# Optimization experiments

Hardware: AMD Instinct MI355X
Metric: run time of the kernel (lower is better)

## Reference

```python
import jax, jax.numpy as jnp
import numpy as np

DIM = 512
NUM_HEADS = 8
HEAD_DIM = DIM // NUM_HEADS


def setup_inputs() -> dict:
    key = jax.random.key(0)
    k1, k2, k3, k4 = jax.random.split(key, 4)
    B, N = 8, 32 * 32
    x = jax.random.normal(k1, (B, N, DIM), dtype=jnp.float32)
    # nn.Linear(dim, 3*dim, bias=False): weight [3*dim, dim], y = x @ W.T
    w_qkv = jax.random.normal(k2, (3 * DIM, DIM), dtype=jnp.float32) * 0.02
    w_proj = jax.random.normal(k3, (DIM, DIM), dtype=jnp.float32) * 0.02
    log_decay = jnp.zeros((NUM_HEADS,), dtype=jnp.float32)
    return {"x": x, "w_qkv": w_qkv, "w_proj": w_proj, "log_decay": log_decay,
            "H": 32, "W": 32}


def _manhattan_dist(H: int, W: int) -> jnp.ndarray:
    # [H*W, H*W] Manhattan distance between grid positions
    rows = jnp.repeat(jnp.arange(H), W)  # [N]
    cols = jnp.tile(jnp.arange(W), H)    # [N]
    dist = (jnp.abs(rows[:, None] - rows[None, :])
            + jnp.abs(cols[:, None] - cols[None, :]))
    return dist.astype(jnp.float32)


def reference(x, w_qkv, w_proj, log_decay, H, W):
    B, N, C = x.shape
    nh, hd = NUM_HEADS, HEAD_DIM
    scale = hd ** -0.5
    qkv = jnp.einsum('bnc,dc->bnd', x, w_qkv)          # [B, N, 3C]
    qkv = qkv.reshape(B, N, 3, nh, hd).transpose(2, 0, 3, 1, 4)
    q, k, v = qkv[0], qkv[1], qkv[2]                   # [B, nh, N, hd]
    attn = jnp.einsum('bhid,bhjd->bhij', q, k) * scale  # [B, nh, N, N]
    dist = _manhattan_dist(H, W)                        # [N, N]
    decay = jax.nn.softplus(log_decay)                  # [nh]
    bias = -decay[:, None, None] * dist[None]           # [nh, N, N]
    attn = jax.nn.softmax(attn + bias[None], axis=-1)
    out = jnp.einsum('bhij,bhjd->bhid', attn, v)        # [B, nh, N, hd]
    out = out.transpose(0, 2, 1, 3).reshape(B, N, C)
    return jnp.einsum('bnc,dc->bnd', out, w_proj)


if __name__ == "__main__":
    out = reference(**setup_inputs())
    print(out.shape, out.dtype)
```

## Files before the change

### kernel.cpp

```cpp
#include <hip/hip_runtime.h>
#include <stdint.h>

typedef _Float16 f16;
typedef _Float16 f16x8 __attribute__((ext_vector_type(8)));
typedef _Float16 f16x4 __attribute__((ext_vector_type(4)));
typedef float f32x4 __attribute__((ext_vector_type(4)));

#define MROWS 8192
#define KDIM 512
#define NSEQ 1024
#define NH 8

__device__ __forceinline__ void gload16(void* lds, const void* g) {
  __builtin_amdgcn_global_load_lds(
      (const __attribute__((address_space(1))) unsigned*)g,
      (__attribute__((address_space(3))) unsigned*)lds, 16, 0, 0);
}

__device__ __forceinline__ f32x4 mfma16(f16x8 a, f16x8 b, f32x4 c) {
  return __builtin_amdgcn_mfma_f32_16x16x32_f16(a, b, c, 0, 0, 0);
}

__device__ __forceinline__ int vsg(int d) {
  return ((d >> 1) & 7) ^ ((d & 1) << 2);
}

__global__ __launch_bounds__(256) void cvt_kernel(
    const float* __restrict__ x, const float* __restrict__ wq,
    const float* __restrict__ wp, f16* __restrict__ x16,
    f16* __restrict__ wq16, f16* __restrict__ wp16) {
  int t = blockIdx.x * 256 + threadIdx.x;
  int stride = gridDim.x * 256;
  for (int i = t; i < (MROWS * KDIM) / 4; i += stride) {
    float4 v = ((const float4*)x)[i];
    f16x4 o = {(f16)v.x, (f16)v.y, (f16)v.z, (f16)v.w};
    ((f16x4*)x16)[i] = o;
  }
  for (int i = t; i < (3 * KDIM * KDIM) / 4; i += stride) {
    float4 v = ((const float4*)wq)[i];
    f16x4 o = {(f16)v.x, (f16)v.y, (f16)v.z, (f16)v.w};
    ((f16x4*)wq16)[i] = o;
  }
  for (int i = t; i < (KDIM * KDIM) / 4; i += stride) {
    float4 v = ((const float4*)wp)[i];
    f16x4 o = {(f16)v.x, (f16)v.y, (f16)v.z, (f16)v.w};
    ((f16x4*)wp16)[i] = o;
  }
}

__device__ __forceinline__ void gemm_mainloop_db(
    const f16* __restrict__ A, const f16* __restrict__ B, int m0, int n0,
    f16* As0, f16* As1, f16* Bs0, f16* Bs1, f32x4 (&acc)[4][4]) {
  const int tid = threadIdx.x;
  const int w = tid >> 6, l = tid & 63;
  const int wr = w >> 1, wc = w & 1;
  const int lrow = l & 15, lk = l >> 4;
  const int srow = l >> 3, sslot = l & 7;
  const int scol = ((sslot ^ srow) << 3);
  const int NT = KDIM / 64;

  auto STAGE = [&](int bb, int kb) {
    f16* Ad = bb ? As1 : As0;
    f16* Bd = bb ? Bs1 : Bs0;
#pragma unroll
    for (int j = 0; j < 4; ++j) {
      int i = w * 4 + j;
      int row = i * 8 + srow;
      gload16(Ad + i * 512, A + (size_t)(m0 + row) * KDIM + kb + scol);
      gload16(Bd + i * 512, B + (size_t)(n0 + row) * KDIM + kb + scol);
    }
  };

  STAGE(0, 0);
#pragma unroll 1
  for (int t = 0; t < NT; ++t) {
    if (t + 1 < NT) {
      STAGE((t + 1) & 1, (t + 1) * 64);
      asm volatile("s_waitcnt vmcnt(8)" ::: "memory");
    } else {
      asm volatile("s_waitcnt vmcnt(0)" ::: "memory");
    }
    __builtin_amdgcn_s_barrier();
    const f16* Asr = (t & 1) ? As1 : As0;
    const f16* Bsr = (t & 1) ? Bs1 : Bs0;
#pragma unroll
    for (int kk = 0; kk < 2; ++kk) {
      int slotbase = kk * 4 + lk;
      f16x8 af[4], bf[4];
#pragma unroll
      for (int mi = 0; mi < 4; ++mi) {
        int row = wr * 64 + mi * 16 + lrow;
        af[mi] = *(const f16x8*)(Asr + row * 64 + ((slotbase ^ (row & 7)) << 3));
      }
#pragma unroll
      for (int nj = 0; nj < 4; ++nj) {
        int row = wc * 64 + nj * 16 + lrow;
        bf[nj] = *(const f16x8*)(Bsr + row * 64 + ((slotbase ^ (row & 7)) << 3));
      }
#pragma unroll
      for (int mi = 0; mi < 4; ++mi)
#pragma unroll
        for (int nj = 0; nj < 4; ++nj)
          acc[mi][nj] = mfma16(af[mi], bf[nj], acc[mi][nj]);
    }
    __builtin_amdgcn_s_barrier();
  }
}

__global__ __launch_bounds__(256, 2) void qkv_gemm(
    const f16* __restrict__ x16, const f16* __restrict__ wq16,
    f16* __restrict__ q16, f16* __restrict__ k16, f16* __restrict__ v16T) {
  __shared__ f16 SMEM[4 * 128 * 64];
  f16* As0 = SMEM;
  f16* As1 = SMEM + 8192;
  f16* Bs0 = SMEM + 16384;
  f16* Bs1 = SMEM + 24576;

  f32x4 acc[4][4];
#pragma unroll
  for (int i = 0; i < 4; ++i)
#pragma unroll
    for (int j = 0; j < 4; ++j) acc[i][j] = (f32x4){0.f, 0.f, 0.f, 0.f};

  const int m0 = blockIdx.y * 128, n0 = blockIdx.x * 128;
  gemm_mainloop_db(x16, wq16, m0, n0, As0, As1, Bs0, Bs1, acc);

  const int tid = threadIdx.x;
  const int w = tid >> 6, l = tid & 63;
  const int wr = w >> 1, wc = w & 1;
  const int lrow = l & 15, lk = l >> 4;

  if (n0 < 1024) {
#pragma unroll
    for (int mi = 0; mi < 4; ++mi) {
#pragma unroll
      for (int rr = 0; rr < 4; ++rr) {
        int m = m0 + wr * 64 + mi * 16 + lk * 4 + rr;
        int b = m >> 10, n = m & 1023;
#pragma unroll
        for (int nj = 0; nj < 4; ++nj) {
          int d = n0 + wc * 64 + nj * 16 + lrow;
          int which = d >> 9, c = d & 511;
          int h = c >> 6, dd = c & 63;
          f16 val = (f16)acc[mi][nj][rr];
          size_t hb = (size_t)(b * NH + h);
          if (which == 0)
            q16[(hb * NSEQ + n) * 64 + dd] = val;
          else
            k16[(hb * NSEQ + n) * 64 + dd] = val;
        }
      }
    }
  } else {
    f16* T = SMEM;
#pragma unroll
    for (int mi = 0; mi < 4; ++mi) {
#pragma unroll
      for (int nj = 0; nj < 4; ++nj) {
        int dloc = wc * 64 + nj * 16 + lrow;
        int nloc = wr * 64 + mi * 16 + lk * 4;
        f16x4 pw = {(f16)acc[mi][nj][0], (f16)acc[mi][nj][1],
                    (f16)acc[mi][nj][2], (f16)acc[mi][nj][3]};
        *(f16x4*)(T + dloc * 136 + nloc) = pw;
      }
    }
    __syncthreads();
    const int b = m0 >> 10;
    const int nbase = m0 & 1023;
#pragma unroll
    for (int rs = 0; rs < 8; ++rs) {
      int dloc = w * 32 + rs * 4 + (l >> 4);
      int ncol = (l & 15) * 8;
      f16x8 vv = *(const f16x8*)(T + dloc * 136 + ncol);
      int c = (n0 + dloc) & 511;
      int hh = c >> 6, dd = c & 63;
      size_t hb = (size_t)(b * NH + hh);
      *(f16x8*)(v16T + (hb * 64 + dd) * NSEQ + nbase + ncol) = vv;
    }
  }
}

__global__ __launch_bounds__(256, 2) void proj_gemm(
    const f16* __restrict__ a16, const f16* __restrict__ wp16,
    float* __restrict__ out) {
  __shared__ f16 As0[128 * 64], As1[128 * 64];
  __shared__ f16 Bs0[128 * 64], Bs1[128 * 64];
  f32x4 acc[4][4];
#pragma unroll
  for (int i = 0; i < 4; ++i)
#pragma unroll
    for (int j = 0; j < 4; ++j) acc[i][j] = (f32x4){0.f, 0.f, 0.f, 0.f};

  const int m0 = blockIdx.y * 128, n0 = blockIdx.x * 128;
  gemm_mainloop_db(a16, wp16, m0, n0, As0, As1, Bs0, Bs1, acc);

  const int tid = threadIdx.x;
  const int w = tid >> 6, l = tid & 63;
  const int wr = w >> 1, wc = w & 1;
#pragma unroll
  for (int mi = 0; mi < 4; ++mi) {
#pragma unroll
    for (int rr = 0; rr < 4; ++rr) {
      int m = m0 + wr * 64 + mi * 16 + (l >> 4) * 4 + rr;
#pragma unroll
      for (int nj = 0; nj < 4; ++nj) {
        int d = n0 + wc * 64 + nj * 16 + (l & 15);
        out[(size_t)m * KDIM + d] = acc[mi][nj][rr];
      }
    }
  }
}

__global__ __launch_bounds__(256, 2) void attn_f16(
    const f16* __restrict__ q16, const f16* __restrict__ k16,
    const f16* __restrict__ v16T, const float* __restrict__ log_decay,
    f16* __restrict__ aout) {
  __shared__ f16 Ks0[64 * 64], Ks1[64 * 64];
  __shared__ f16 Vt0[64 * 64], Vt1[64 * 64];
  __shared__ f16 Ps0[128 * 64], Ps1[128 * 64];

  const int tid = threadIdx.x;
  const int w = tid >> 6, l = tid & 63;
  const int lrow = l & 15, lk = l >> 4;
  const int srow = l >> 3, sslot = l & 7;

  const int L = blockIdx.x;
  const int pair = (L & 7) * 8 + ((L >> 3) & 7);
  const int q0 = (L >> 6) * 128;
  const int b = pair >> 3, h = pair & 7;

  const size_t kbase = ((size_t)(b * NH + h)) * NSEQ * 64;
  const size_t vbase = ((size_t)(b * NH + h)) * 64 * NSEQ;

  const float decay = log1pf(__expf(log_decay[h]));
  const float negdecay = -decay;

  f16x8 qf[2][2];
#pragma unroll
  for (int njq = 0; njq < 2; ++njq)
#pragma unroll
    for (int kk = 0; kk < 2; ++kk) {
      int row = q0 + w * 32 + njq * 16 + lrow;
      f16x8 v = *(const f16x8*)(q16 + kbase + (size_t)row * 64 + kk * 32 + lk * 8);
#pragma unroll
      for (int e = 0; e < 8; ++e) v[e] = v[e] * (f16)0.125f;
      qf[njq][kk] = v;
    }

  int qr_[2], qc_[2];
#pragma unroll
  for (int njq = 0; njq < 2; ++njq) {
    int qn = q0 + w * 32 + njq * 16 + lrow;
    qr_[njq] = qn >> 5;
    qc_[njq] = qn & 31;
  }

  float bdc[2][4][4];
#pragma unroll
  for (int njq = 0; njq < 2; ++njq)
#pragma unroll
    for (int mi = 0; mi < 4; ++mi)
#pragma unroll
      for (int rr = 0; rr < 4; ++rr) {
        int kc = (mi * 16 + lk * 4 + rr) & 31;
        int da = qc_[njq] - kc;
        da = (da < 0) ? -da : da;
        bdc[njq][mi][rr] = negdecay * (float)da;
      }

  f32x4 O[2][4];
#pragma unroll
  for (int njq = 0; njq < 2; ++njq)
#pragma unroll
    for (int dj = 0; dj < 4; ++dj) O[njq][dj] = (f32x4){0.f, 0.f, 0.f, 0.f};
  float mrow[2] = {-1e30f, -1e30f}, lsum[2] = {0.f, 0.f};

  auto STAGE = [&](int bb, int cc0) {
    f16* Kd = bb ? Ks1 : Ks0;
    f16* Vd = bb ? Vt1 : Vt0;
#pragma unroll
    for (int j = 0; j < 2; ++j) {
      int i = w * 2 + j;
      int row = i * 8 + srow;
      gload16(Kd + i * 512,
              k16 + kbase + (size_t)(cc0 + row) * 64 + ((sslot ^ (row & 7)) << 3));
      gload16(Vd + i * 512,
              v16T + vbase + (size_t)row * NSEQ + cc0 + ((sslot ^ vsg(row)) << 3));
    }
  };

  STAGE(0, 0);
#pragma unroll 1
  for (int t = 0; t < NSEQ / 64; ++t) {
    const int c0 = t * 64;
    const int cur = t & 1;
    asm volatile("s_waitcnt vmcnt(0)" ::: "memory");
    __builtin_amdgcn_s_barrier();
    if (t + 1 < NSEQ / 64) STAGE(cur ^ 1, c0 + 64);

    const f16* Kc = cur ? Ks1 : Ks0;
    const f16* Vc = cur ? Vt1 : Vt0;
    f16* Psc = cur ? Ps1 : Ps0;

    f32x4 s[4][2];
#pragma unroll
    for (int mi = 0; mi < 4; ++mi)
#pragma unroll
      for (int njq = 0; njq < 2; ++njq) s[mi][njq] = (f32x4){0.f, 0.f, 0.f, 0.f};
#pragma unroll
    for (int kk = 0; kk < 2; ++kk) {
#pragma unroll
      for (int mi = 0; mi < 4; ++mi) {
        int row = mi * 16 + lrow;
        f16x8 kf = *(const f16x8*)(Kc + row * 64 + (((kk * 4 + lk) ^ (row & 7)) << 3));
#pragma unroll
        for (int njq = 0; njq < 2; ++njq)
          s[mi][njq] = mfma16(kf, qf[njq][kk], s[mi][njq]);
      }
    }

    float bdr[2][2];
#pragma unroll
    for (int njq = 0; njq < 2; ++njq) {
      int d0 = qr_[njq] - 2 * t;
      int a0 = (d0 < 0) ? -d0 : d0;
      int d1 = d0 - 1;
      int a1 = (d1 < 0) ? -d1 : d1;
      bdr[njq][0] = negdecay * (float)a0;
      bdr[njq][1] = negdecay * (float)a1;
    }

    float al[2];
#pragma unroll
    for (int njq = 0; njq < 2; ++njq) {
      float mx = -1e30f;
#pragma unroll
      for (int mi = 0; mi < 4; ++mi) {
        float bdrm = bdr[njq][mi >> 1];
#pragma unroll
        for (int rr = 0; rr < 4; ++rr) {
          float tt = s[mi][njq][rr] + (bdc[njq][mi][rr] + bdrm);
          s[mi][njq][rr] = tt;
          mx = fmaxf(mx, tt);
        }
      }
      mx = fmaxf(mx, __shfl_xor(mx, 16));
      mx = fmaxf(mx, __shfl_xor(mx, 32));
      float mnew = fmaxf(mrow[njq], mx);
      al[njq] = __expf(mrow[njq] - mnew);
      mrow[njq] = mnew;
      float rs = 0.f;
      int qq = w * 32 + njq * 16 + lrow;
#pragma unroll
      for (int mi = 0; mi < 4; ++mi) {
        f16x4 pw;
#pragma unroll
        for (int rr = 0; rr < 4; ++rr) {
          float p = __expf(s[mi][njq][rr] - mnew);
          rs += p;
          pw[rr] = (f16)p;
        }
        int slot = mi * 2 + (lk >> 1);
        *(f16x4*)(Psc + qq * 64 + ((slot ^ (qq & 7)) << 3) + ((lk & 1) << 2)) = pw;
      }
      rs += __shfl_xor(rs, 16);
      rs += __shfl_xor(rs, 32);
      lsum[njq] = lsum[njq] * al[njq] + rs;
    }

#pragma unroll
    for (int njq = 0; njq < 2; ++njq) {
#pragma unroll
      for (int rr = 0; rr < 4; ++rr) {
        float a = __shfl(al[njq], lk * 4 + rr);
#pragma unroll
        for (int dj = 0; dj < 4; ++dj) O[njq][dj][rr] *= a;
      }
    }

    asm volatile("s_waitcnt lgkmcnt(0)" ::: "memory");
    __builtin_amdgcn_s_barrier();

#pragma unroll
    for (int kk = 0; kk < 2; ++kk) {
      int slotbase = kk * 4 + lk;
      f16x8 pa[2], vb[4];
#pragma unroll
      for (int njq = 0; njq < 2; ++njq) {
        int row = w * 32 + njq * 16 + lrow;
        pa[njq] = *(const f16x8*)(Psc + row * 64 + ((slotbase ^ (row & 7)) << 3));
      }
#pragma unroll
      for (int dj = 0; dj < 4; ++dj) {
        int d = dj * 16 + lrow;
        vb[dj] = *(const f16x8*)(Vc + d * 64 + ((slotbase ^ vsg(d)) << 3));
      }
#pragma unroll
      for (int njq = 0; njq < 2; ++njq)
#pragma unroll
        for (int dj = 0; dj < 4; ++dj)
          O[njq][dj] = mfma16(pa[njq], vb[dj], O[njq][dj]);
    }
  }

  float linv[2] = {1.f / lsum[0], 1.f / lsum[1]};
#pragma unroll
  for (int njq = 0; njq < 2; ++njq) {
#pragma unroll
    for (int rr = 0; rr < 4; ++rr) {
      float inv = __shfl(linv[njq], lk * 4 + rr);
      int qn = q0 + w * 32 + njq * 16 + lk * 4 + rr;
      size_t rowbase = ((size_t)(b * NSEQ + qn)) * KDIM + h * 64;
#pragma unroll
      for (int dj = 0; dj < 4; ++dj)
        aout[rowbase + dj * 16 + lrow] = (f16)(O[njq][dj][rr] * inv);
    }
  }
}

extern "C" void kernel_launch(void* const* d_in, const int* in_sizes, int n_in,
                              void* d_out, int out_size, void* d_ws, size_t ws_size,
                              hipStream_t stream) {
  const float* x = (const float*)d_in[0];
  const float* w_qkv = (const float*)d_in[1];
  const float* w_proj = (const float*)d_in[2];
  const float* log_decay = (const float*)d_in[3];

  f16* ws = (f16*)d_ws;
  f16* x16 = ws;
  f16* wq16 = x16 + (size_t)MROWS * KDIM;
  f16* wp16 = wq16 + (size_t)3 * KDIM * KDIM;
  f16* q16 = wp16 + (size_t)KDIM * KDIM;
  f16* k16 = q16 + (size_t)MROWS * KDIM;
  f16* v16T = k16 + (size_t)MROWS * KDIM;
  f16* a16 = v16T + (size_t)MROWS * KDIM;

  cvt_kernel<<<1024, 256, 0, stream>>>(x, w_qkv, w_proj, x16, wq16, wp16);
  qkv_gemm<<<dim3(12, 64), 256, 0, stream>>>(x16, wq16, q16, k16, v16T);
  attn_f16<<<dim3(512), 256, 0, stream>>>(q16, k16, v16T, log_decay, a16);
  proj_gemm<<<dim3(4, 64), 256, 0, stream>>>(a16, wp16, (float*)d_out);
}
```

Before: 146.4 us.

## Retile proj GEMM, use exp2 with lazy rescaling, and single-buffer P in attention

The projection GEMM gets its own main loop with 128x64 tiles and twice as many blocks, plus a partial vmcnt wait so the next-stage load overlaps compute. The attention kernel folds log2(e) into the Q scale and decay so it can use exp2f, and rescales the running max and output only when the max grows by more than a threshold. It also drops the double-buffered P tile and the barrier before the PV stage, and adds s_setprio around the MFMA sections. Removing that barrier may be safe because each wave writes and reads only its own P rows, but the lazy-max threshold lets P values exceed 1 in f16, which trades some numerical headroom for fewer rescales.

```diff
diff --git a/kernel.cpp b/kernel.cpp
--- a/kernel.cpp
+++ b/kernel.cpp
@@ -10,6 +10,7 @@
 #define KDIM 512
 #define NSEQ 1024
 #define NH 8
+#define LOG2E 1.44269504f
 
 __device__ __forceinline__ void gload16(void* lds, const void* g) {
   __builtin_amdgcn_global_load_lds(
@@ -184,27 +185,81 @@
     const f16* __restrict__ a16, const f16* __restrict__ wp16,
     float* __restrict__ out) {
   __shared__ f16 As0[128 * 64], As1[128 * 64];
-  __shared__ f16 Bs0[128 * 64], Bs1[128 * 64];
-  f32x4 acc[4][4];
+  __shared__ f16 Bs0[64 * 64], Bs1[64 * 64];
+  f32x4 acc[4][2];
 #pragma unroll
   for (int i = 0; i < 4; ++i)
 #pragma unroll
-    for (int j = 0; j < 4; ++j) acc[i][j] = (f32x4){0.f, 0.f, 0.f, 0.f};
-
-  const int m0 = blockIdx.y * 128, n0 = blockIdx.x * 128;
-  gemm_mainloop_db(a16, wp16, m0, n0, As0, As1, Bs0, Bs1, acc);
-
+    for (int j = 0; j < 2; ++j) acc[i][j] = (f32x4){0.f, 0.f, 0.f, 0.f};
+
+  const int m0 = blockIdx.y * 128, n0 = blockIdx.x * 64;
   const int tid = threadIdx.x;
   const int w = tid >> 6, l = tid & 63;
   const int wr = w >> 1, wc = w & 1;
+  const int lrow = l & 15, lk = l >> 4;
+  const int srow = l >> 3, sslot = l & 7;
+  const int scol = ((sslot ^ srow) << 3);
+
+  auto STAGE = [&](int bb, int kb) {
+    f16* Ad = bb ? As1 : As0;
+    f16* Bd = bb ? Bs1 : Bs0;
+#pragma unroll
+    for (int j = 0; j < 4; ++j) {
+      int i = w * 4 + j;
+      int row = i * 8 + srow;
+      gload16(Ad + i * 512, a16 + (size_t)(m0 + row) * KDIM + kb + scol);
+    }
+#pragma unroll
+    for (int j = 0; j < 2; ++j) {
+      int i = w * 2 + j;
+      int row = i * 8 + srow;
+      gload16(Bd + i * 512, wp16 + (size_t)(n0 + row) * KDIM + kb + scol);
+    }
+  };
+
+  STAGE(0, 0);
+#pragma unroll 1
+  for (int t = 0; t < KDIM / 64; ++t) {
+    if (t + 1 < KDIM / 64) {
+      STAGE((t + 1) & 1, (t + 1) * 64);
+      asm volatile("s_waitcnt vmcnt(6)" ::: "memory");
+    } else {
+      asm volatile("s_waitcnt vmcnt(0)" ::: "memory");
+    }
+    __builtin_amdgcn_s_barrier();
+    const f16* Asr = (t & 1) ? As1 : As0;
+    const f16* Bsr = (t & 1) ? Bs1 : Bs0;
+#pragma unroll
+    for (int kk = 0; kk < 2; ++kk) {
+      int slotbase = kk * 4 + lk;
+      f16x8 af[4], bf[2];
+#pragma unroll
+      for (int mi = 0; mi < 4; ++mi) {
+        int row = wr * 64 + mi * 16 + lrow;
+        af[mi] = *(const f16x8*)(Asr + row * 64 + ((slotbase ^ (row & 7)) << 3));
+      }
+#pragma unroll
+      for (int nj = 0; nj < 2; ++nj) {
+        int row = wc * 32 + nj * 16 + lrow;
+        bf[nj] = *(const f16x8*)(Bsr + row * 64 + ((slotbase ^ (row & 7)) << 3));
+      }
+#pragma unroll
+      for (int mi = 0; mi < 4; ++mi)
+#pragma unroll
+        for (int nj = 0; nj < 2; ++nj)
+          acc[mi][nj] = mfma16(af[mi], bf[nj], acc[mi][nj]);
+    }
+    __builtin_amdgcn_s_barrier();
+  }
+
 #pragma unroll
   for (int mi = 0; mi < 4; ++mi) {
 #pragma unroll
     for (int rr = 0; rr < 4; ++rr) {
-      int m = m0 + wr * 64 + mi * 16 + (l >> 4) * 4 + rr;
-#pragma unroll
-      for (int nj = 0; nj < 4; ++nj) {
-        int d = n0 + wc * 64 + nj * 16 + (l & 15);
+      int m = m0 + wr * 64 + mi * 16 + lk * 4 + rr;
+#pragma unroll
+      for (int nj = 0; nj < 2; ++nj) {
+        int d = n0 + wc * 32 + nj * 16 + lrow;
         out[(size_t)m * KDIM + d] = acc[mi][nj][rr];
       }
     }
@@ -217,7 +272,7 @@
     f16* __restrict__ aout) {
   __shared__ f16 Ks0[64 * 64], Ks1[64 * 64];
   __shared__ f16 Vt0[64 * 64], Vt1[64 * 64];
-  __shared__ f16 Ps0[128 * 64], Ps1[128 * 64];
+  __shared__ f16 Ps[128 * 64];
 
   const int tid = threadIdx.x;
   const int w = tid >> 6, l = tid & 63;
@@ -232,8 +287,8 @@
   const size_t kbase = ((size_t)(b * NH + h)) * NSEQ * 64;
   const size_t vbase = ((size_t)(b * NH + h)) * 64 * NSEQ;
 
-  const float decay = log1pf(__expf(log_decay[h]));
-  const float negdecay = -decay;
+  const float decay2 = log1pf(__expf(log_decay[h])) * LOG2E;
+  const float negdecay = -decay2;
 
   f16x8 qf[2][2];
 #pragma unroll
@@ -243,7 +298,7 @@
       int row = q0 + w * 32 + njq * 16 + lrow;
       f16x8 v = *(const f16x8*)(q16 + kbase + (size_t)row * 64 + kk * 32 + lk * 8);
 #pragma unroll
-      for (int e = 0; e < 8; ++e) v[e] = v[e] * (f16)0.125f;
+      for (int e = 0; e < 8; ++e) v[e] = v[e] * (f16)(0.125f * LOG2E);
       qf[njq][kk] = v;
     }
 
@@ -292,21 +347,20 @@
   STAGE(0, 0);
 #pragma unroll 1
   for (int t = 0; t < NSEQ / 64; ++t) {
-    const int c0 = t * 64;
     const int cur = t & 1;
     asm volatile("s_waitcnt vmcnt(0)" ::: "memory");
     __builtin_amdgcn_s_barrier();
-    if (t + 1 < NSEQ / 64) STAGE(cur ^ 1, c0 + 64);
+    if (t + 1 < NSEQ / 64) STAGE(cur ^ 1, t * 64 + 64);
 
     const f16* Kc = cur ? Ks1 : Ks0;
     const f16* Vc = cur ? Vt1 : Vt0;
-    f16* Psc = cur ? Ps1 : Ps0;
 
     f32x4 s[4][2];
 #pragma unroll
     for (int mi = 0; mi < 4; ++mi)
 #pragma unroll
       for (int njq = 0; njq < 2; ++njq) s[mi][njq] = (f32x4){0.f, 0.f, 0.f, 0.f};
+    __builtin_amdgcn_s_setprio(1);
 #pragma unroll
     for (int kk = 0; kk < 2; ++kk) {
 #pragma unroll
@@ -318,6 +372,7 @@
           s[mi][njq] = mfma16(kf, qf[njq][kk], s[mi][njq]);
       }
     }
+    __builtin_amdgcn_s_setprio(0);
 
     float bdr[2][2];
 #pragma unroll
@@ -330,7 +385,6 @@
       bdr[njq][1] = negdecay * (float)a1;
     }
 
-    float al[2];
 #pragma unroll
     for (int njq = 0; njq < 2; ++njq) {
       float mx = -1e30f;
@@ -346,9 +400,18 @@
       }
       mx = fmaxf(mx, __shfl_xor(mx, 16));
       mx = fmaxf(mx, __shfl_xor(mx, 32));
-      float mnew = fmaxf(mrow[njq], mx);
-      al[njq] = __expf(mrow[njq] - mnew);
-      mrow[njq] = mnew;
+      if (__any(mx > mrow[njq] + 8.f)) {
+        float mnew = fmaxf(mrow[njq], mx);
+        float a = exp2f(mrow[njq] - mnew);
+        mrow[njq] = mnew;
+        lsum[njq] *= a;
+#pragma unroll
+        for (int rr = 0; rr < 4; ++rr) {
+          float av = __shfl(a, lk * 4 + rr);
+#pragma unroll
+          for (int dj = 0; dj < 4; ++dj) O[njq][dj][rr] *= av;
+        }
+      }
       float rs = 0.f;
       int qq = w * 32 + njq * 16 + lrow;
 #pragma unroll
@@ -356,31 +419,21 @@
         f16x4 pw;
 #pragma unroll
         for (int rr = 0; rr < 4; ++rr) {
-          float p = __expf(s[mi][njq][rr] - mnew);
+          float p = exp2f(s[mi][njq][rr] - mrow[njq]);
           rs += p;
           pw[rr] = (f16)p;
         }
         int slot = mi * 2 + (lk >> 1);
-        *(f16x4*)(Psc + qq * 64 + ((slot ^ (qq & 7)) << 3) + ((lk & 1) << 2)) = pw;
+        *(f16x4*)(Ps + qq * 64 + ((slot ^ (qq & 7)) << 3) + ((lk & 1) << 2)) = pw;
       }
       rs += __shfl_xor(rs, 16);
       rs += __shfl_xor(rs, 32);
-      lsum[njq] = lsum[njq] * al[njq] + rs;
-    }
-
-#pragma unroll
-    for (int njq = 0; njq < 2; ++njq) {
-#pragma unroll
-      for (int rr = 0; rr < 4; ++rr) {
-        float a = __shfl(al[njq], lk * 4 + rr);
-#pragma unroll
-        for (int dj = 0; dj < 4; ++dj) O[njq][dj][rr] *= a;
-      }
+      lsum[njq] += rs;
     }
 
     asm volatile("s_waitcnt lgkmcnt(0)" ::: "memory");
-    __builtin_amdgcn_s_barrier();
-
+
+    __builtin_amdgcn_s_setprio(1);
 #pragma unroll
     for (int kk = 0; kk < 2; ++kk) {
       int slotbase = kk * 4 + lk;
@@ -388,7 +441,7 @@
 #pragma unroll
       for (int njq = 0; njq < 2; ++njq) {
         int row = w * 32 + njq * 16 + lrow;
-        pa[njq] = *(const f16x8*)(Psc + row * 64 + ((slotbase ^ (row & 7)) << 3));
+        pa[njq] = *(const f16x8*)(Ps + row * 64 + ((slotbase ^ (row & 7)) << 3));
       }
 #pragma unroll
       for (int dj = 0; dj < 4; ++dj) {
@@ -401,6 +454,7 @@
         for (int dj = 0; dj < 4; ++dj)
           O[njq][dj] = mfma16(pa[njq], vb[dj], O[njq][dj]);
     }
+    __builtin_amdgcn_s_setprio(0);
   }
 
   float linv[2] = {1.f / lsum[0], 1.f / lsum[1]};
@@ -438,5 +492,5 @@
   cvt_kernel<<<1024, 256, 0, stream>>>(x, w_qkv, w_proj, x16, wq16, wp16);
   qkv_gemm<<<dim3(12, 64), 256, 0, stream>>>(x16, wq16, q16, k16, v16T);
   attn_f16<<<dim3(512), 256, 0, stream>>>(q16, k16, v16T, log_decay, a16);
-  proj_gemm<<<dim3(4, 64), 256, 0, stream>>>(a16, wp16, (float*)d_out);
-}
+  proj_gemm<<<dim3(8, 64), 256, 0, stream>>>(a16, wp16, (float*)d_out);
+}
```

After: 153.1 us. +4.6%, slower.
